# Kernel optimization log

Measured on AMD Instinct MI355X. Metric: run time of the kernel, lower is better.

The kernel has to match this reference:

```python
import jax, jax.numpy as jnp
import numpy as np

B, S, H, NH, HD, FF = 2, 2048, 2048, 16, 128, 8192
EPS = 1e-05
THETA = 10000.0


def _rms(x, w):
    return x * jax.lax.rsqrt(jnp.mean(x * x, axis=-1, keepdims=True) + EPS) * w


def _rope(q, k):
    # q,k: [b, h, s, d]; standard rotate-half RoPE with positions 0..s-1
    s, hd = q.shape[2], q.shape[3]
    inv = 1.0 / (THETA ** (jnp.arange(0, hd, 2, dtype=jnp.float32) / hd))
    f = jnp.arange(s, dtype=jnp.float32)[:, None] * inv[None, :]   # [s, d/2]
    cos = jnp.concatenate([jnp.cos(f), jnp.cos(f)], axis=-1)       # [s, d]
    sin = jnp.concatenate([jnp.sin(f), jnp.sin(f)], axis=-1)
    rot = lambda x: jnp.concatenate([-x[..., hd // 2:], x[..., :hd // 2]], axis=-1)
    return q * cos + rot(q) * sin, k * cos + rot(k) * sin


def _highway(x, w, g, gb):
    # sigmoid(W_g x + b) * (W_h x)
    return jax.nn.sigmoid(x @ g.T + gb) * (x @ w.T)


def setup_inputs() -> dict:
    key = jax.random.key(0)
    ks = jax.random.split(key, 16)
    n = lambda i, shape, s=0.02: jax.random.normal(ks[i], shape, dtype=jnp.float32) * s
    return dict(
        x_mod=n(0, (B, S, H), 1.0),
        x_back=n(1, (B, S, H), 1.0),
        mask=jnp.zeros((1, 1, S, S), jnp.float32),
        wq=n(2, (H, H)), wk=n(3, (H, H)), wv=n(4, (H, H)), wo=n(5, (H, H)),
        cross_ln_w=jnp.ones((H,), jnp.float32),
        fb_w=n(6, (H, H)), fb_g=n(7, (H, H)), fb_gb=jnp.zeros((H,), jnp.float32),
        dr_w=n(8, (H, H)), dr_g=n(9, (H, H)), dr_gb=jnp.zeros((H,), jnp.float32),
        in_ln_w=jnp.ones((H,), jnp.float32),
        post_ln_w=jnp.ones((H,), jnp.float32),
        w_gate=n(10, (FF, H)), w_up=n(11, (FF, H)), w_down=n(12, (H, FF)),
    )


def reference(x_mod, x_back, mask, wq, wk, wv, wo, cross_ln_w,
              fb_w, fb_g, fb_gb, dr_w, dr_g, dr_gb,
              in_ln_w, post_ln_w, w_gate, w_up, w_down):
    b, s, _ = x_mod.shape
    scale = HD ** -0.5

    # feedback highway on x_mod (returned as delta)
    delta = _highway(x_mod, fb_w, fb_g, fb_gb)

    # cross-attention: q from RMSNorm(x_mod), k/v from x_back
    qn = _rms(x_mod, cross_ln_w)
    split = lambda t: t.reshape(b, s, NH, HD).transpose(0, 2, 1, 3)  # [b,h,s,d]
    qh = split(qn @ wq.T)
    kh = split(x_back @ wk.T)
    vh = split(x_back @ wv.T)
    qh, kh = _rope(qh, kh)

    attn = jnp.einsum('bhqd,bhkd->bhqk', qh, kh) * scale + mask
    attn = jax.nn.softmax(attn, axis=-1)  # dropout is identity in eval
    out = jnp.einsum('bhqk,bhkd->bhqd', attn, vh)
    out = out.transpose(0, 2, 1, 3).reshape(b, s, NH * HD)
    mod = out @ wo.T

    # driver highway on x_back
    drv = _highway(x_back, dr_w, dr_g, dr_gb)

    x = x_mod + mod + drv

    # delegated LLaMA-style decoder layer with self_attn == Identity:
    # x = x + Identity(RMSNorm(x)); then x = x + SwiGLU_MLP(RMSNorm(x))
    x = x + _rms(x, in_ln_w)
    h = _rms(x, post_ln_w)
    mlp = (jax.nn.silu(h @ w_gate.T) * (h @ w_up.T)) @ w_down.T
    x = x + mlp

    return (x, delta)
```

## Files before the change

kernel.cpp:

```cpp
#include <hip/hip_runtime.h>
#include <cstdint>
#include <cstddef>

#define H_DIM 2048
#define S_LEN 2048
#define B_SZ  2
#define NH_N  16
#define HD_D  128
#define FF_D  8192
#define T_TOK (B_SZ * S_LEN)
#define MB (size_t)(1 << 20)

typedef __bf16 bf16x8 __attribute__((ext_vector_type(8)));
typedef float  f32x4  __attribute__((ext_vector_type(4)));

__device__ __forceinline__ float bf2f(unsigned short u) {
  unsigned int x = ((unsigned int)u) << 16;
  float f;
  __builtin_memcpy(&f, &x, 4);
  return f;
}
__device__ __forceinline__ unsigned short f2bf(float f) {
  unsigned int x;
  __builtin_memcpy(&x, &f, 4);
  x += 0x7fffu + ((x >> 16) & 1u);
  return (unsigned short)(x >> 16);
}
__device__ __forceinline__ f32x4 mfma16(bf16x8 a, bf16x8 b, f32x4 c) {
  return __builtin_amdgcn_mfma_f32_16x16x32_bf16(a, b, c, 0, 0, 0);
}
__device__ __forceinline__ bf16x8 lds8(const unsigned short* p) {
  return *reinterpret_cast<const bf16x8*>(p);
}
__device__ __forceinline__ void gll16(const unsigned short* g, unsigned short* l) {
  __builtin_amdgcn_global_load_lds(
      (__attribute__((address_space(1))) unsigned int*)(g),
      (__attribute__((address_space(3))) unsigned int*)(l), 16, 0, 0);
}
__device__ __forceinline__ float sigm(float x) { return 1.0f / (1.0f + __expf(-x)); }

__global__ __launch_bounds__(256) void cast_k(const float* __restrict__ in,
                                              unsigned short* __restrict__ o, int n8) {
  const int i = blockIdx.x * 256 + threadIdx.x;
  if (i >= n8) return;
  const size_t base = (size_t)i * 8;
  const float4* p = reinterpret_cast<const float4*>(in + base);
  float4 a = p[0], b = p[1];
  unsigned short ov[8];
  ov[0] = f2bf(a.x); ov[1] = f2bf(a.y); ov[2] = f2bf(a.z); ov[3] = f2bf(a.w);
  ov[4] = f2bf(b.x); ov[5] = f2bf(b.y); ov[6] = f2bf(b.z); ov[7] = f2bf(b.w);
  *reinterpret_cast<uint4*>(o + base) = *(const uint4*)ov;
}

template <int MODE>
__global__ __launch_bounds__(256, 2) void gemm_bt(
    const unsigned short* __restrict__ A, const unsigned short* __restrict__ W,
    void* __restrict__ Cv, const float* __restrict__ Add, int M, int N, int K) {
  __shared__ unsigned short As[128 * 32];
  __shared__ unsigned short Bs[128 * 32];

  const int t    = threadIdx.x;
  const int lane = t & 63;
  const int wave = t >> 6;
  const int lr   = lane & 15;
  const int quad = lane >> 4;
  const int wr   = wave >> 1;
  const int wc   = wave & 1;
  const int row0 = blockIdx.y * 128;
  const int col0 = blockIdx.x * 128;

  const unsigned short* a0 = A + (size_t)(row0 + (t >> 2)) * K + (t & 3) * 8;
  const unsigned short* b0 = W + (size_t)(col0 + (t >> 2)) * K + (t & 3) * 8;
  const size_t k64 = (size_t)64 * K;

  unsigned short* lA0 = &As[t * 8];
  unsigned short* lA1 = &As[2048 + t * 8];
  unsigned short* lB0 = &Bs[t * 8];
  unsigned short* lB1 = &Bs[2048 + t * 8];

  f32x4 acc[4][4];
#pragma unroll
  for (int i = 0; i < 4; ++i)
#pragma unroll
    for (int j = 0; j < 4; ++j) acc[i][j] = (f32x4){0.f, 0.f, 0.f, 0.f};

  for (int kt = 0; kt < K; kt += 32) {
    gll16(a0 + kt, lA0);
    gll16(a0 + kt + k64, lA1);
    gll16(b0 + kt, lB0);
    gll16(b0 + kt + k64, lB1);
    __syncthreads();

    bf16x8 af[4], bfr[4];
#pragma unroll
    for (int i = 0; i < 4; ++i)
      af[i] = lds8(&As[(wr * 64 + i * 16 + lr) * 32 + quad * 8]);
#pragma unroll
    for (int j = 0; j < 4; ++j)
      bfr[j] = lds8(&Bs[(wc * 64 + j * 16 + lr) * 32 + quad * 8]);
#pragma unroll
    for (int i = 0; i < 4; ++i)
#pragma unroll
      for (int j = 0; j < 4; ++j) acc[i][j] = mfma16(af[i], bfr[j], acc[i][j]);
    __syncthreads();
  }

#pragma unroll
  for (int i = 0; i < 4; ++i) {
    const int r0 = row0 + wr * 64 + i * 16 + quad * 4;
#pragma unroll
    for (int j = 0; j < 4; ++j) {
      const int c = col0 + wc * 64 + j * 16 + lr;
      const size_t base = (size_t)r0 * N + c;
      f32x4 v = acc[i][j];
#pragma unroll
      for (int r = 0; r < 4; ++r) {
        if (MODE == 0) {
          ((unsigned short*)Cv)[base + (size_t)r * N] = f2bf(v[r]);
        } else {
          ((float*)Cv)[base + (size_t)r * N] = v[r] + Add[base + (size_t)r * N];
        }
      }
    }
  }
}

template <int OUTBF, int ADDX>
__global__ __launch_bounds__(256) void rms_k(const float* __restrict__ x,
                                             const float* __restrict__ w,
                                             void* __restrict__ o) {
  const int row = blockIdx.x;
  const int t = threadIdx.x;
  const float* xr = x + (size_t)row * H_DIM;

  const float4* xp = reinterpret_cast<const float4*>(xr) + t * 2;
  float4 a = xp[0], b = xp[1];
  float f[8] = {a.x, a.y, a.z, a.w, b.x, b.y, b.z, b.w};
  float ss = 0.f;
#pragma unroll
  for (int m = 0; m < 8; ++m) ss += f[m] * f[m];
#pragma unroll
  for (int off = 32; off > 0; off >>= 1) ss += __shfl_xor(ss, off);
  __shared__ float red[4];
  if ((t & 63) == 0) red[t >> 6] = ss;
  __syncthreads();
  const float tot = red[0] + red[1] + red[2] + red[3];
  const float inv = 1.0f / sqrtf(tot * (1.0f / H_DIM) + 1e-5f);

  const float4* wp = reinterpret_cast<const float4*>(w) + t * 2;
  float4 wa = wp[0], wb = wp[1];
  float wv[8] = {wa.x, wa.y, wa.z, wa.w, wb.x, wb.y, wb.z, wb.w};

  if (OUTBF) {
    unsigned short ov[8];
#pragma unroll
    for (int m = 0; m < 8; ++m) ov[m] = f2bf(f[m] * inv * wv[m]);
    reinterpret_cast<uint4*>((unsigned short*)o + (size_t)row * H_DIM)[t] = *(const uint4*)ov;
  } else {
    float ov[8];
#pragma unroll
    for (int m = 0; m < 8; ++m) {
      float r = f[m] * inv * wv[m];
      ov[m] = ADDX ? (f[m] + r) : r;
    }
    float4* op = reinterpret_cast<float4*>((float*)o + (size_t)row * H_DIM) + t * 2;
    op[0] = *(const float4*)&ov[0];
    op[1] = *(const float4*)&ov[4];
  }
}

__global__ __launch_bounds__(256) void rope_k(unsigned short* __restrict__ q,
                                              unsigned short* __restrict__ k) {
  const int idx  = blockIdx.x * 256 + threadIdx.x;
  const int i    = idx & 63;
  const int head = (idx >> 6) & (NH_N - 1);
  const int tok  = idx >> 10;
  const int pos  = tok & (S_LEN - 1);

  const float inv = expf(-(float)i * (9.210340371976184f / 64.0f));
  const float ang = (float)pos * inv;
  const float c = cosf(ang), s = sinf(ang);

  const size_t base = (size_t)tok * H_DIM + head * HD_D;
  float q1 = bf2f(q[base + i]),      q2 = bf2f(q[base + i + 64]);
  float k1 = bf2f(k[base + i]),      k2 = bf2f(k[base + i + 64]);
  q[base + i]      = f2bf(q1 * c - q2 * s);
  q[base + i + 64] = f2bf(q2 * c + q1 * s);
  k[base + i]      = f2bf(k1 * c - k2 * s);
  k[base + i + 64] = f2bf(k2 * c + k1 * s);
}

__device__ __forceinline__ int vt_off(int d, int key) {
  return d * 72 + (((key >> 3) ^ ((d >> 3) & 7)) << 3) + (key & 7);
}

__global__ __launch_bounds__(256, 2) void attn_k(const unsigned short* __restrict__ q,
                                                 const unsigned short* __restrict__ kk,
                                                 const unsigned short* __restrict__ vv,
                                                 unsigned short* __restrict__ o) {
  const int bh = blockIdx.y;
  const int b = bh >> 4, h = bh & 15;
  const int q0 = blockIdx.x * 64;
  const int t = threadIdx.x;
  const int lane = t & 63, wave = t >> 6;
  const int lr = lane & 15, quad = lane >> 4;
  const float scale = 0.08838834764831845f;

  __shared__ unsigned short Ks[64 * 136];
  __shared__ unsigned short VT[128 * 72];
  __shared__ unsigned short Pw[4][16 * 72];

  const size_t qrow = (size_t)(b * S_LEN + q0 + wave * 16 + lr);
  const unsigned short* qbase = q + qrow * H_DIM + h * HD_D;
  bf16x8 qf[4];
#pragma unroll
  for (int c = 0; c < 4; ++c)
    qf[c] = *reinterpret_cast<const bf16x8*>(qbase + c * 32 + quad * 8);

  f32x4 accO[8];
#pragma unroll
  for (int d = 0; d < 8; ++d) accO[d] = (f32x4){0.f, 0.f, 0.f, 0.f};
  float mrow[4] = {-1e30f, -1e30f, -1e30f, -1e30f};
  float lrow[4] = {0.f, 0.f, 0.f, 0.f};

  const unsigned short* kbase = kk + (size_t)(b * S_LEN) * H_DIM + h * HD_D;
  const unsigned short* vbase = vv + (size_t)(b * S_LEN) * H_DIM + h * HD_D;

  for (int kv = 0; kv < S_LEN; kv += 64) {
#pragma unroll
    for (int it = 0; it < 4; ++it) {
      const int idx = it * 256 + t;
      const int key = idx >> 4;
      const int d0 = (idx & 15) * 8;
      uint4 kvv = *reinterpret_cast<const uint4*>(kbase + (size_t)(kv + key) * H_DIM + d0);
      *reinterpret_cast<uint4*>(&Ks[key * 136 + d0]) = kvv;
      uint4 vvv = *reinterpret_cast<const uint4*>(vbase + (size_t)(kv + key) * H_DIM + d0);
      const unsigned short* vp = (const unsigned short*)&vvv;
#pragma unroll
      for (int m = 0; m < 8; ++m) VT[vt_off(d0 + m, key)] = vp[m];
    }
    __syncthreads();

    f32x4 sc[4];
#pragma unroll
    for (int kt = 0; kt < 4; ++kt) sc[kt] = (f32x4){0.f, 0.f, 0.f, 0.f};
#pragma unroll
    for (int kt = 0; kt < 4; ++kt)
#pragma unroll
      for (int c = 0; c < 4; ++c) {
        bf16x8 bfr = lds8(&Ks[(kt * 16 + lr) * 136 + c * 32 + quad * 8]);
        sc[kt] = mfma16(qf[c], bfr, sc[kt]);
      }

    float alpha[4];
#pragma unroll
    for (int r = 0; r < 4; ++r) {
      float mx = sc[0][r];
      mx = fmaxf(mx, sc[1][r]); mx = fmaxf(mx, sc[2][r]); mx = fmaxf(mx, sc[3][r]);
      mx *= scale;
#pragma unroll
      for (int off = 1; off < 16; off <<= 1) mx = fmaxf(mx, __shfl_xor(mx, off));
      const float mnew = fmaxf(mrow[r], mx);
      alpha[r] = __expf(mrow[r] - mnew);
      float sum = 0.f;
#pragma unroll
      for (int kt = 0; kt < 4; ++kt) {
        float p = __expf(sc[kt][r] * scale - mnew);
        Pw[wave][(quad * 4 + r) * 72 + kt * 16 + lr] = f2bf(p);
        sum += p;
      }
#pragma unroll
      for (int off = 1; off < 16; off <<= 1) sum += __shfl_xor(sum, off);
      lrow[r] = lrow[r] * alpha[r] + sum;
      mrow[r] = mnew;
    }
#pragma unroll
    for (int d = 0; d < 8; ++d)
#pragma unroll
      for (int r = 0; r < 4; ++r) accO[d][r] *= alpha[r];

    bf16x8 ap[2];
#pragma unroll
    for (int c = 0; c < 2; ++c)
      ap[c] = lds8(&Pw[wave][lr * 72 + c * 32 + quad * 8]);
#pragma unroll
    for (int dt = 0; dt < 8; ++dt)
#pragma unroll
      for (int c = 0; c < 2; ++c) {
        bf16x8 bfr = lds8(&VT[vt_off(dt * 16 + lr, c * 32 + quad * 8)]);
        accO[dt] = mfma16(ap[c], bfr, accO[dt]);
      }
    __syncthreads();
  }

#pragma unroll
  for (int r = 0; r < 4; ++r) {
    const float invl = 1.0f / lrow[r];
    const size_t orow = (size_t)(b * S_LEN + q0 + wave * 16 + quad * 4 + r);
#pragma unroll
    for (int dt = 0; dt < 8; ++dt)
      o[orow * H_DIM + h * HD_D + dt * 16 + lr] = f2bf(accO[dt][r] * invl);
  }
}

__global__ __launch_bounds__(256) void highway_k(const unsigned short* __restrict__ G,
                                                 const unsigned short* __restrict__ Wx,
                                                 const float* __restrict__ gb,
                                                 float* __restrict__ o) {
  const size_t i8 = (size_t)blockIdx.x * 256 + threadIdx.x;
  const size_t base = i8 * 8;
  const int col = (int)(base & (H_DIM - 1));
  uint4 gv = *reinterpret_cast<const uint4*>(G + base);
  uint4 wv = *reinterpret_cast<const uint4*>(Wx + base);
  const float4* bp = reinterpret_cast<const float4*>(gb + col);
  float4 b0 = bp[0], b1 = bp[1];
  float bb[8] = {b0.x, b0.y, b0.z, b0.w, b1.x, b1.y, b1.z, b1.w};
  const unsigned short *ge = (const unsigned short*)&gv, *we = (const unsigned short*)&wv;
  float ov[8];
#pragma unroll
  for (int m = 0; m < 8; ++m)
    ov[m] = sigm(bf2f(ge[m]) + bb[m]) * bf2f(we[m]);
  float4* op = reinterpret_cast<float4*>(o + base);
  op[0] = *(const float4*)&ov[0];
  op[1] = *(const float4*)&ov[4];
}

__global__ __launch_bounds__(256) void combine_k(const float* __restrict__ xm,
                                                 const unsigned short* __restrict__ mod,
                                                 const unsigned short* __restrict__ G,
                                                 const unsigned short* __restrict__ Wx,
                                                 const float* __restrict__ gb,
                                                 float* __restrict__ o) {
  const size_t i8 = (size_t)blockIdx.x * 256 + threadIdx.x;
  const size_t base = i8 * 8;
  const int col = (int)(base & (H_DIM - 1));
  const float4* xp = reinterpret_cast<const float4*>(xm + base);
  float4 x0 = xp[0], x1 = xp[1];
  float xx[8] = {x0.x, x0.y, x0.z, x0.w, x1.x, x1.y, x1.z, x1.w};
  uint4 mv = *reinterpret_cast<const uint4*>(mod + base);
  uint4 gv = *reinterpret_cast<const uint4*>(G + base);
  uint4 wv = *reinterpret_cast<const uint4*>(Wx + base);
  const float4* bp = reinterpret_cast<const float4*>(gb + col);
  float4 b0 = bp[0], b1 = bp[1];
  float bb[8] = {b0.x, b0.y, b0.z, b0.w, b1.x, b1.y, b1.z, b1.w};
  const unsigned short *me = (const unsigned short*)&mv, *ge = (const unsigned short*)&gv,
                       *we = (const unsigned short*)&wv;
  float ov[8];
#pragma unroll
  for (int m = 0; m < 8; ++m) {
    float drv = sigm(bf2f(ge[m]) + bb[m]) * bf2f(we[m]);
    ov[m] = xx[m] + bf2f(me[m]) + drv;
  }
  float4* op = reinterpret_cast<float4*>(o + base);
  op[0] = *(const float4*)&ov[0];
  op[1] = *(const float4*)&ov[4];
}

__global__ __launch_bounds__(256) void silumul_k(const unsigned short* __restrict__ G,
                                                 const unsigned short* __restrict__ U,
                                                 unsigned short* __restrict__ o) {
  const size_t i8 = (size_t)blockIdx.x * 256 + threadIdx.x;
  const size_t base = i8 * 8;
  uint4 gv = *reinterpret_cast<const uint4*>(G + base);
  uint4 uv = *reinterpret_cast<const uint4*>(U + base);
  const unsigned short *ge = (const unsigned short*)&gv, *ue = (const unsigned short*)&uv;
  unsigned short ov[8];
#pragma unroll
  for (int m = 0; m < 8; ++m) {
    float g = bf2f(ge[m]);
    ov[m] = f2bf(g * sigm(g) * bf2f(ue[m]));
  }
  *reinterpret_cast<uint4*>(o + base) = *(const uint4*)ov;
}

static inline void cast_f2b(const float* in, unsigned short* o, size_t n, hipStream_t st) {
  int n8 = (int)(n / 8);
  cast_k<<<(n8 + 255) / 256, 256, 0, st>>>(in, o, n8);
}
static inline void launch_gemm(const void* A, const void* W, void* C,
                               int M, int N, int K, hipStream_t st) {
  dim3 grid(N / 128, M / 128), blk(256);
  gemm_bt<0><<<grid, blk, 0, st>>>((const unsigned short*)A, (const unsigned short*)W,
                                   C, nullptr, M, N, K);
}

extern "C" void kernel_launch(void* const* d_in, const int* in_sizes, int n_in,
                              void* d_out, int out_size, void* d_ws, size_t ws_size,
                              hipStream_t stream) {
  const float* x_mod      = (const float*)d_in[0];
  const float* x_back     = (const float*)d_in[1];
  const float* wq         = (const float*)d_in[3];
  const float* wk         = (const float*)d_in[4];
  const float* wv         = (const float*)d_in[5];
  const float* wo         = (const float*)d_in[6];
  const float* cross_ln_w = (const float*)d_in[7];
  const float* fb_w       = (const float*)d_in[8];
  const float* fb_g       = (const float*)d_in[9];
  const float* fb_gb      = (const float*)d_in[10];
  const float* dr_w       = (const float*)d_in[11];
  const float* dr_g       = (const float*)d_in[12];
  const float* dr_gb      = (const float*)d_in[13];
  const float* in_ln_w    = (const float*)d_in[14];
  const float* post_ln_w  = (const float*)d_in[15];
  const float* w_gate     = (const float*)d_in[16];
  const float* w_up       = (const float*)d_in[17];
  const float* w_down     = (const float*)d_in[18];

  float* out = (float*)d_out;

  char* w = (char*)d_ws;
  unsigned short* xb0 = (unsigned short*)(w);
  unsigned short* xb1 = (unsigned short*)(w + 16 * MB);
  unsigned short* wb[8];
  for (int i = 0; i < 8; ++i) wb[i] = (unsigned short*)(w + 32 * MB + (size_t)i * 8 * MB);
  unsigned short* wgb = (unsigned short*)(w + 96 * MB);
  unsigned short* wub = (unsigned short*)(w + 128 * MB);
  unsigned short* wdb = (unsigned short*)(w + 160 * MB);
  unsigned short* s0  = (unsigned short*)(w + 192 * MB);
  unsigned short* s1  = (unsigned short*)(w + 208 * MB);
  unsigned short* s2  = (unsigned short*)(w + 224 * MB);
  unsigned short* s3  = (unsigned short*)(w + 240 * MB);
  float*          xf  = (float*)(w + 256 * MB);
  float*          x2f = (float*)(w + 288 * MB);
  unsigned short* f0  = (unsigned short*)(w + 320 * MB);
  unsigned short* f1  = (unsigned short*)(w + 32 * MB);

  const size_t HH = (size_t)H_DIM * H_DIM;
  const size_t FH = (size_t)FF_D * H_DIM;
  const size_t TH = (size_t)T_TOK * H_DIM;

  cast_f2b(x_mod,  xb0,  TH, stream);
  cast_f2b(x_back, xb1,  TH, stream);
  cast_f2b(fb_g,   wb[0], HH, stream);
  cast_f2b(fb_w,   wb[1], HH, stream);
  cast_f2b(wq,     wb[2], HH, stream);
  cast_f2b(wk,     wb[3], HH, stream);
  cast_f2b(wv,     wb[4], HH, stream);
  cast_f2b(wo,     wb[5], HH, stream);
  cast_f2b(dr_g,   wb[6], HH, stream);
  cast_f2b(dr_w,   wb[7], HH, stream);
  cast_f2b(w_gate, wgb,  FH, stream);
  cast_f2b(w_up,   wub,  FH, stream);
  cast_f2b(w_down, wdb,  FH, stream);

  const int ETH = (int)(TH / 8 / 256);
  const int EFF = (int)((size_t)T_TOK * FF_D / 8 / 256);

  launch_gemm(xb0, wb[0], s0, T_TOK, H_DIM, H_DIM, stream);
  launch_gemm(xb0, wb[1], s1, T_TOK, H_DIM, H_DIM, stream);
  highway_k<<<ETH, 256, 0, stream>>>(s0, s1, fb_gb, out + TH);

  rms_k<1, 0><<<T_TOK, 256, 0, stream>>>(x_mod, cross_ln_w, s2);
  launch_gemm(s2, wb[2], s0, T_TOK, H_DIM, H_DIM, stream);
  launch_gemm(xb1, wb[3], s1, T_TOK, H_DIM, H_DIM, stream);
  launch_gemm(xb1, wb[4], s3, T_TOK, H_DIM, H_DIM, stream);

  rope_k<<<T_TOK * NH_N * 64 / 256, 256, 0, stream>>>(s0, s1);

  attn_k<<<dim3(S_LEN / 64, B_SZ * NH_N), 256, 0, stream>>>(s0, s1, s3, s2);

  launch_gemm(s2, wb[5], s0, T_TOK, H_DIM, H_DIM, stream);

  launch_gemm(xb1, wb[6], s1, T_TOK, H_DIM, H_DIM, stream);
  launch_gemm(xb1, wb[7], s3, T_TOK, H_DIM, H_DIM, stream);
  combine_k<<<ETH, 256, 0, stream>>>(x_mod, s0, s1, s3, dr_gb, xf);

  rms_k<0, 1><<<T_TOK, 256, 0, stream>>>(xf, in_ln_w, x2f);
  rms_k<1, 0><<<T_TOK, 256, 0, stream>>>(x2f, post_ln_w, s1);

  launch_gemm(s1, wgb, f0, T_TOK, FF_D, H_DIM, stream);
  launch_gemm(s1, wub, f1, T_TOK, FF_D, H_DIM, stream);
  silumul_k<<<EFF, 256, 0, stream>>>(f0, f1, f0);

  gemm_bt<1><<<dim3(H_DIM / 128, T_TOK / 128), 256, 0, stream>>>(
      f0, wdb, out, x2f, T_TOK, H_DIM, FF_D);

  (void)in_sizes; (void)n_in; (void)out_size; (void)ws_size;
}
```

Measured before the change: 1.778 ms.

## Prefetch K/V tiles with async global-to-LDS loads and XOR-swizzled LDS layout in attention

```diff
diff --git a/kernel.cpp b/kernel.cpp
--- a/kernel.cpp
+++ b/kernel.cpp
@@ -190,25 +190,23 @@
   k[base + i + 64] = f2bf(k2 * c + k1 * s);
 }
 
-__device__ __forceinline__ int vt_off(int d, int key) {
-  return d * 72 + (((key >> 3) ^ ((d >> 3) & 7)) << 3) + (key & 7);
-}
-
-__global__ __launch_bounds__(256, 2) void attn_k(const unsigned short* __restrict__ q,
+__global__ __launch_bounds__(256, 4) void attn_k(const unsigned short* __restrict__ q,
                                                  const unsigned short* __restrict__ kk,
                                                  const unsigned short* __restrict__ vv,
                                                  unsigned short* __restrict__ o) {
-  const int bh = blockIdx.y;
+  const int lb  = blockIdx.y * gridDim.x + blockIdx.x;
+  const int sid = ((lb & 7) << 7) | (lb >> 3);
+  const int bh  = sid >> 5;
   const int b = bh >> 4, h = bh & 15;
-  const int q0 = blockIdx.x * 64;
+  const int q0 = (sid & 31) * 64;
   const int t = threadIdx.x;
   const int lane = t & 63, wave = t >> 6;
   const int lr = lane & 15, quad = lane >> 4;
   const float scale = 0.08838834764831845f;
 
-  __shared__ unsigned short Ks[64 * 136];
-  __shared__ unsigned short VT[128 * 72];
-  __shared__ unsigned short Pw[4][16 * 72];
+  __shared__ unsigned short Ks[64 * 128];
+  __shared__ unsigned short VT[128 * 64];
+  __shared__ unsigned short Pw[4 * 16 * 64];
 
   const size_t qrow = (size_t)(b * S_LEN + q0 + wave * 16 + lr);
   const unsigned short* qbase = q + qrow * H_DIM + h * HD_D;
@@ -226,47 +224,75 @@
   const unsigned short* kbase = kk + (size_t)(b * S_LEN) * H_DIM + h * HD_D;
   const unsigned short* vbase = vv + (size_t)(b * S_LEN) * H_DIM + h * HD_D;
 
+  uint4 vpre[4];
+#pragma unroll
+  for (int it = 0; it < 4; ++it) {
+    const int idx = it * 256 + t;
+    const int key = idx >> 4;
+    const int d0  = (idx & 15) * 8;
+    gll16(kbase + (size_t)key * H_DIM + (d0 ^ ((key & 7) << 3)), &Ks[(size_t)idx * 8]);
+    vpre[it] = *reinterpret_cast<const uint4*>(vbase + (size_t)key * H_DIM + d0);
+  }
+
   for (int kv = 0; kv < S_LEN; kv += 64) {
 #pragma unroll
     for (int it = 0; it < 4; ++it) {
       const int idx = it * 256 + t;
       const int key = idx >> 4;
-      const int d0 = (idx & 15) * 8;
-      uint4 kvv = *reinterpret_cast<const uint4*>(kbase + (size_t)(kv + key) * H_DIM + d0);
-      *reinterpret_cast<uint4*>(&Ks[key * 136 + d0]) = kvv;
-      uint4 vvv = *reinterpret_cast<const uint4*>(vbase + (size_t)(kv + key) * H_DIM + d0);
-      const unsigned short* vp = (const unsigned short*)&vvv;
-#pragma unroll
-      for (int m = 0; m < 8; ++m) VT[vt_off(d0 + m, key)] = vp[m];
+      const int d0  = (idx & 15) * 8;
+      const unsigned short* vp = (const unsigned short*)&vpre[it];
+#pragma unroll
+      for (int m = 0; m < 8; ++m) {
+        const int row = d0 + m;
+        const int sw  = (row ^ (row >> 3)) & 7;
+        *(unsigned short*)((char*)VT + row * 128 + ((key * 2) ^ (sw << 4))) = vp[m];
+      }
     }
     __syncthreads();
 
+    const int nkv = kv + 64;
+    if (nkv < S_LEN) {
+#pragma unroll
+      for (int it = 0; it < 4; ++it) {
+        const int idx = it * 256 + t;
+        const int d0  = (idx & 15) * 8;
+        vpre[it] = *reinterpret_cast<const uint4*>(
+            vbase + (size_t)(nkv + (idx >> 4)) * H_DIM + d0);
+      }
+    }
+
     f32x4 sc[4];
 #pragma unroll
     for (int kt = 0; kt < 4; ++kt) sc[kt] = (f32x4){0.f, 0.f, 0.f, 0.f};
+    __builtin_amdgcn_s_setprio(1);
 #pragma unroll
     for (int kt = 0; kt < 4; ++kt)
 #pragma unroll
       for (int c = 0; c < 4; ++c) {
-        bf16x8 bfr = lds8(&Ks[(kt * 16 + lr) * 136 + c * 32 + quad * 8]);
+        const int row = kt * 16 + lr;
+        bf16x8 bfr = *(const bf16x8*)((const char*)Ks + row * 256 +
+                                      ((c * 64 + quad * 16) ^ ((row & 7) << 4)));
         sc[kt] = mfma16(qf[c], bfr, sc[kt]);
       }
+    __builtin_amdgcn_s_setprio(0);
 
     float alpha[4];
 #pragma unroll
     for (int r = 0; r < 4; ++r) {
-      float mx = sc[0][r];
-      mx = fmaxf(mx, sc[1][r]); mx = fmaxf(mx, sc[2][r]); mx = fmaxf(mx, sc[3][r]);
+      float mx = fmaxf(fmaxf(sc[0][r], sc[1][r]), fmaxf(sc[2][r], sc[3][r]));
       mx *= scale;
 #pragma unroll
       for (int off = 1; off < 16; off <<= 1) mx = fmaxf(mx, __shfl_xor(mx, off));
       const float mnew = fmaxf(mrow[r], mx);
       alpha[r] = __expf(mrow[r] - mnew);
+      const int prow = quad * 4 + r;
+      const int psw  = (prow ^ (prow >> 3)) & 7;
       float sum = 0.f;
 #pragma unroll
       for (int kt = 0; kt < 4; ++kt) {
         float p = __expf(sc[kt][r] * scale - mnew);
-        Pw[wave][(quad * 4 + r) * 72 + kt * 16 + lr] = f2bf(p);
+        *(unsigned short*)((char*)Pw + wave * 2048 + prow * 128 +
+                           (((kt * 16 + lr) * 2) ^ (psw << 4))) = f2bf(p);
         sum += p;
       }
 #pragma unroll
@@ -282,15 +308,32 @@
     bf16x8 ap[2];
 #pragma unroll
     for (int c = 0; c < 2; ++c)
-      ap[c] = lds8(&Pw[wave][lr * 72 + c * 32 + quad * 8]);
+      ap[c] = *(const bf16x8*)((const char*)Pw + wave * 2048 + lr * 128 +
+                               ((c * 64 + quad * 16) ^ (((lr ^ (lr >> 3)) & 7) << 4)));
+    __builtin_amdgcn_s_setprio(1);
 #pragma unroll
     for (int dt = 0; dt < 8; ++dt)
 #pragma unroll
       for (int c = 0; c < 2; ++c) {
-        bf16x8 bfr = lds8(&VT[vt_off(dt * 16 + lr, c * 32 + quad * 8)]);
+        const int row = dt * 16 + lr;
+        const int sw  = (row ^ (row >> 3)) & 7;
+        bf16x8 bfr = *(const bf16x8*)((const char*)VT + row * 128 +
+                                      ((c * 64 + quad * 16) ^ (sw << 4)));
         accO[dt] = mfma16(ap[c], bfr, accO[dt]);
       }
+    __builtin_amdgcn_s_setprio(0);
     __syncthreads();
+
+    if (nkv < S_LEN) {
+#pragma unroll
+      for (int it = 0; it < 4; ++it) {
+        const int idx  = it * 256 + t;
+        const int krow = idx >> 4;
+        const int d0   = (idx & 15) * 8;
+        gll16(kbase + (size_t)(nkv + krow) * H_DIM + (d0 ^ ((krow & 7) << 3)),
+              &Ks[(size_t)idx * 8]);
+      }
+    }
   }
 
 #pragma unroll
```

Measured after the change: 2.050 ms. +15.3%, slower.
